# Optimization experiments

Hardware: AMD Instinct MI355X
Metric: run time of the kernel (lower is better)

Reference implementation:

```python
import jax, jax.numpy as jnp
import numpy as np

N, E = 50000, 800000        # nodes, edges
L, MUL, S = 2, 32, 5        # layers, irrep multiplicity, num_species
NB, H = 8, 64               # num_bessel, radial MLP hidden
R_MAX = 5.0
AVG_NEIGH = 16.0
NW = 4 * MUL                # radial-MLP output size: 4 uvu TP paths x mul


def _envelope(x, p=6):
    # polynomial cutoff envelope u(x), smoothly -> 0 at x=1
    u = (1.0
         - (p + 1.0) * (p + 2.0) / 2.0 * x ** p
         + p * (p + 2.0) * x ** (p + 1)
         - p * (p + 1.0) / 2.0 * x ** (p + 2))
    return u * (x < 1.0)


def _forward(edge_vectors, node_species, senders, receivers, embed_w,
             w_res_s, w_res_v, w_lin1_s, w_lin1_v, mlp_w0, mlp_w1, mlp_w2,
             w_lin2_s, w_lin2_v, w_out1, w_out2):
    r = jnp.sqrt(jnp.sum(edge_vectors ** 2, -1) + 1e-12)            # [E] safe_norm
    unit = edge_vectors / r[:, None]
    sh1 = jnp.sqrt(3.0) * unit                                      # l=1 SH, component norm [E,3]
    # Bessel radial basis * polynomial envelope -> edge embedding [E,NB]
    n = jnp.arange(1, NB + 1, dtype=jnp.float32)
    bessel = jnp.sqrt(2.0 / R_MAX) * jnp.sin(n[None, :] * jnp.pi * r[:, None] / R_MAX) / r[:, None]
    edge_embedded = bessel * _envelope(r / R_MAX)[:, None]

    onehot = jax.nn.one_hot(node_species, S, dtype=jnp.float32)     # [N,S] node attrs (Sx0e)
    h_s = (onehot @ embed_w) / jnp.sqrt(S)                          # [N,MUL] 0e features
    h_v = jnp.zeros((N, MUL, 3), jnp.float32)                       # [N,MUL,3] 1o features (no path from 0e attrs)

    for l in range(L):
        # residual: FullyConnectedTensorProduct(node_feats, node_attrs) into h_out irreps
        res_s = jnp.einsum('nu,ns,usk->nk', h_s, onehot, w_res_s[l]) / jnp.sqrt(MUL * S)   # [N,2*MUL] (feat+gate scalars)
        res_v = jnp.einsum('nui,ns,usv->nvi', h_v, onehot, w_res_v[l]) / jnp.sqrt(MUL * S) # [N,MUL,3]
        # self-interaction Linear (per-irrep channel mixing)
        hs = (h_s @ w_lin1_s[l]) / jnp.sqrt(MUL)
        hv = jnp.einsum('nui,uv->nvi', h_v, w_lin1_v[l]) / jnp.sqrt(MUL)
        # gather sender node features onto edges
        es, ev = hs[senders], hv[senders]                           # [E,MUL], [E,MUL,3]
        # radial MLP (swish, no bias) -> per-edge uvu TP path weights [E, 4*MUL]
        a = jax.nn.silu(edge_embedded @ (mlp_w0[l] / jnp.sqrt(NB)))
        a = jax.nn.silu(a @ (mlp_w1[l] / jnp.sqrt(H)))
        w = a @ mlp_w2[l]
        w1, w2, w3, w4 = jnp.split(w, 4, axis=-1)
        # per-edge Clebsch-Gordan tensor product, uvu mode, radial weights
        o0a = w1 * es                                               # 0e x 0e -> 0e
        o0b = w2 * jnp.einsum('eui,ei->eu', ev, sh1) / jnp.sqrt(3.0)  # 1o x 1o -> 0e
        o1a = (w3 * es)[:, :, None] * sh1[:, None, :]               # 0e x 1o -> 1o
        o1b = w4[:, :, None] * ev                                   # 1o x 0e -> 1o
        # scatter-sum to receiver nodes + neighbor normalization
        seg = lambda x: jax.ops.segment_sum(x, receivers, num_segments=N) / AVG_NEIGH
        n0 = jnp.concatenate([seg(o0a), seg(o0b)], axis=-1)         # [N,2*MUL]
        n1 = jnp.concatenate([seg(o1a), seg(o1b)], axis=1)          # [N,2*MUL,3]
        # Linear to h_out irreps, add residual
        s_out = n0 @ w_lin2_s[l] / jnp.sqrt(2 * MUL) + res_s        # [N,2*MUL]
        v_out = jnp.einsum('nui,uv->nvi', n1, w_lin2_v[l]) / jnp.sqrt(2 * MUL) + res_v
        # gated nonlinearity: swish on even scalars, swish-activated gates scale vectors
        h_s = jax.nn.silu(s_out[:, :MUL])
        h_v = v_out * jax.nn.silu(s_out[:, MUL:])[:, :, None]
    # scalar readout: MUL -> MUL//2 -> 1 per node
    z = (h_s @ w_out1) / jnp.sqrt(MUL)
    e_node = (z @ w_out2) / jnp.sqrt(MUL // 2)
    return jnp.ravel(e_node)                                        # [N]


def setup_inputs():
    key = jax.random.key(0)
    ks = jax.random.split(key, 16)
    return {
        "edge_vectors": jax.random.normal(ks[0], (E, 3), jnp.float32) * 2.0,
        "node_species": jax.random.randint(ks[1], (N,), 0, S),
        "senders": jax.random.randint(ks[2], (E,), 0, N),
        "receivers": jax.random.randint(ks[3], (E,), 0, N),
        "embed_w": jax.random.normal(ks[4], (S, MUL), jnp.float32),
        "w_res_s": jax.random.normal(ks[5], (L, MUL, S, 2 * MUL), jnp.float32),
        "w_res_v": jax.random.normal(ks[6], (L, MUL, S, MUL), jnp.float32),
        "w_lin1_s": jax.random.normal(ks[7], (L, MUL, MUL), jnp.float32),
        "w_lin1_v": jax.random.normal(ks[8], (L, MUL, MUL), jnp.float32),
        "mlp_w0": jax.random.normal(ks[9], (L, NB, H), jnp.float32) * 4.0,
        "mlp_w1": jax.random.normal(ks[10], (L, H, H), jnp.float32) * 4.0,
        "mlp_w2": jax.random.normal(ks[11], (L, H, NW), jnp.float32) * 4.0 / np.sqrt(H),
        "w_lin2_s": jax.random.normal(ks[12], (L, 2 * MUL, 2 * MUL), jnp.float32),
        "w_lin2_v": jax.random.normal(ks[13], (L, 2 * MUL, MUL), jnp.float32),
        "w_out1": jax.random.normal(ks[14], (MUL, MUL // 2), jnp.float32),
        "w_out2": jax.random.normal(ks[15], (MUL // 2, 1), jnp.float32),
    }


def reference(edge_vectors, node_species, senders, receivers, embed_w,
              w_res_s, w_res_v, w_lin1_s, w_lin1_v, mlp_w0, mlp_w1, mlp_w2,
              w_lin2_s, w_lin2_v, w_out1, w_out2):
    return _forward(edge_vectors, node_species, senders, receivers, embed_w,
                    w_res_s, w_res_v, w_lin1_s, w_lin1_v, mlp_w0, mlp_w1, mlp_w2,
                    w_lin2_s, w_lin2_v, w_out1, w_out2)
```

## Files before the change

kernel.cpp:

```cpp
#include <hip/hip_runtime.h>
#include <math.h>

#define NN 50000
#define EE 800000
#define TB 4096

typedef float f32x2 __attribute__((ext_vector_type(2)));
typedef float f32x4  __attribute__((ext_vector_type(4)));

__device__ __forceinline__ float silu_f(float x) {
    return x / (1.f + __expf(-x));
}

__global__ __launch_bounds__(256) void k_table(
        const float* __restrict__ mlp_w0, const float* __restrict__ mlp_w1,
        const float* __restrict__ mlp_w2,
        float* __restrict__ tab0, float* __restrict__ tab1) {
    __shared__ float stage[4][128];
    int wv = threadIdx.x >> 6, lane = threadIdx.x & 63;
    int wid = blockIdx.x * 4 + wv;
    if (wid > 2 * TB + 1) wid = 2 * TB + 1;
    int l = wid / (TB + 1);
    int bin = wid - l * (TB + 1);
    float* st = stage[wv];

    float r = 5.f * (float)bin / (float)TB;
    if (r < 1e-6f) r = 1e-6f;
    float ir = 1.f / r;
    float xx = r * 0.2f;
    float env = 0.f;
    if (xx < 1.f) {
        float x2 = xx * xx, x3 = x2 * xx, x6 = x3 * x3, x7 = x6 * xx, x8 = x7 * xx;
        env = 1.f - 28.f * x6 + 48.f * x7 - 21.f * x8;
    }
    float coef = 0.6324555320336759f * env * ir;
    const float w5 = 0.6283185307179586f;

    float p = 0.f;
#pragma unroll
    for (int k = 0; k < 8; ++k)
        p += coef * __sinf(w5 * (float)(k + 1) * r) * mlp_w0[l * 512 + k * 64 + lane];
    float a1 = silu_f(p * 0.35355339059327373f);
    st[lane] = a1;
    __syncthreads();
    float q = 0.f;
    for (int j = 0; j < 64; ++j) q += st[j] * mlp_w1[l * 4096 + j * 64 + lane];
    float a2 = silu_f(q * 0.125f);
    __syncthreads();
    st[lane] = a2;
    __syncthreads();
    float wlo = 0.f, whi = 0.f;
    for (int h = 0; h < 64; ++h) {
        float a = st[h];
        wlo += a * mlp_w2[l * 8192 + h * 128 + lane];
        whi += a * mlp_w2[l * 8192 + h * 128 + 64 + lane];
    }
    __syncthreads();
    st[lane] = wlo;
    st[64 + lane] = whi;
    __syncthreads();
    if (lane < 16) {
        f32x4 o;
        if (l == 0) {
            o[0] = st[lane]; o[1] = st[64 + lane];
            o[2] = st[16 + lane]; o[3] = st[80 + lane];
            ((f32x4*)tab0)[bin * 16 + lane] = o;
        } else {
            o[0] = st[lane]; o[1] = st[32 + lane];
            o[2] = st[16 + lane]; o[3] = st[48 + lane];
            ((f32x4*)tab1)[bin * 16 + lane] = o;
        }
    }
}

__global__ void k_fs(const float* __restrict__ embed_w, const float* __restrict__ w_lin1_s,
                     float* __restrict__ fs) {
    int t = threadIdx.x;
    if (t >= 160) return;
    int sp = t >> 5, v = t & 31;
    float acc = 0.f;
#pragma unroll
    for (int u = 0; u < 32; ++u) acc += embed_w[sp * 32 + u] * w_lin1_s[u * 32 + v];
    fs[t] = acc * 0.4472135954999579f * 0.17677669529663687f;
}

__global__ void k_hist(const int* __restrict__ recv, int* __restrict__ deg) {
    int e = blockIdx.x * 256 + threadIdx.x;
    if (e < EE) atomicAdd(&deg[recv[e]], 1);
}

__global__ void k_scan(const int* __restrict__ deg, int* __restrict__ row_start,
                       int* __restrict__ cursor) {
    __shared__ int part[256];
    int t = threadIdx.x;
    int lo = t * 196, hi = lo + 196 > NN ? NN : lo + 196;
    int s = 0;
    for (int i = lo; i < hi; ++i) s += deg[i];
    part[t] = s;
    __syncthreads();
    for (int d = 1; d < 256; d <<= 1) {
        int add = (t >= d) ? part[t - d] : 0;
        __syncthreads();
        part[t] += add;
        __syncthreads();
    }
    int run = part[t] - s;
    for (int i = lo; i < hi; ++i) {
        row_start[i] = run;
        cursor[i] = run;
        run += deg[i];
    }
    if (t == 255) row_start[NN] = run;
}

__global__ void k_fill(const int* __restrict__ recv, const int* __restrict__ senders,
                       const int* __restrict__ species, const float* __restrict__ evec,
                       int* __restrict__ cursor,
                       int* __restrict__ csr_send, int* __restrict__ csr_recv,
                       float* __restrict__ ev3) {
    int e = blockIdx.x * 256 + threadIdx.x;
    if (e >= EE) return;
    int rv = recv[e];
    int p = atomicAdd(&cursor[rv], 1);
    int snd = senders[e];
    csr_send[p] = snd | (species[snd] << 24);
    csr_recv[p] = rv;
    ev3[p * 3 + 0] = evec[e * 3 + 0];
    ev3[p * 3 + 1] = evec[e * 3 + 1];
    ev3[p * 3 + 2] = evec[e * 3 + 2];
}

#define WROWS 20
#define WSTRIDE 260
template<int L>
__global__ __launch_bounds__(256) void k_mega(
    const int* __restrict__ csr_send, const int* __restrict__ csr_recv,
    const float* __restrict__ ev3, const int* __restrict__ row_start,
    const float* __restrict__ fs, const float* __restrict__ feat,
    const float* __restrict__ tab,
    float* __restrict__ n0, float* __restrict__ n1) {
    __shared__ f32x4 accw4[WROWS * WSTRIDE / 4];
    __shared__ f32x4 lds_esh[256];
    __shared__ float lds_x[256];
    __shared__ int lds_wd[256];
    __shared__ int sh_base, sh_last;
    float* accw = (float*)accw4;

    int tid = threadIdx.x;
    int p0 = blockIdx.x * 256;
    int lane = tid & 63;
    int wv = tid >> 6;
    int c0 = lane & 15;
    int rg = lane >> 4;

    for (int i = tid; i < WROWS * WSTRIDE / 4; i += 256) accw4[i] = (f32x4)0.f;

    int sndp = csr_send[p0 + tid];
    int rv = csr_recv[p0 + tid];
    if (tid == 0)   sh_base = rv;
    if (tid == 255) sh_last = rv;
    {
        float x = ev3[(p0 + tid) * 3 + 0], y = ev3[(p0 + tid) * 3 + 1], z = ev3[(p0 + tid) * 3 + 2];
        float r = sqrtf(x * x + y * y + z * z + 1e-12f);
        float ir = 1.f / r;
        const float s3 = 1.7320508075688772f;
        f32x4 esh;
        esh[0] = s3 * x * ir;
        esh[1] = s3 * y * ir;
        esh[2] = s3 * z * ir;
        esh[3] = __int_as_float(sndp);
        lds_esh[tid] = esh;
        float xb = r * ((float)TB / 5.f);
        if (xb > (float)TB) xb = (float)TB;
        lds_x[tid] = xb;
    }
    __syncthreads();
    int node_base = sh_base;
    lds_wd[tid] = rv - node_base;

    const f32x4* tabv = (const f32x4*)tab;
    const f32x4* feat4 = (const f32x4*)feat;
    const float rs3 = 0.5773502691896258f;

    for (int t = 0; t < 4; ++t) {
        int tOff = wv * 64 + t * 16;

        f32x4 eshv[4], dv[4];
        int wr[4];
        float es0[4], es1[4];
#pragma unroll
        for (int j = 0; j < 4; ++j) {
            int idx = tOff + rg * 4 + j;
            eshv[j] = lds_esh[idx];
            wr[j] = lds_wd[idx];
            float xb = lds_x[idx];
            int bin = (int)xb;
            if (bin >= TB) bin = TB - 1;
            float fr = xb - (float)bin;
            f32x4 lo = tabv[bin * 16 + c0];
            f32x4 hi = tabv[bin * 16 + 16 + c0];
            dv[j] = lo + fr * (hi - lo);
            if (L == 0) {
                int sp = ((unsigned)__float_as_int(eshv[j][3])) >> 24;
                es0[j] = fs[sp * 32 + c0];
                es1[j] = fs[sp * 32 + 16 + c0];
            }
        }

#pragma unroll
        for (int b = 0; b < 2; ++b) {
            int u = b * 16 + c0;
            float s0 = 0.f, s1 = 0.f, s2 = 0.f, s3v = 0.f;
            int curw = wr[0];
            auto emit = [&](int wrow) {
                if (L == 0) {
                    if (wrow < WROWS) {
                        float* arow = accw + wrow * WSTRIDE;
                        atomicAdd(arow + u, s0);
                        atomicAdd(arow + 64 + u, s1);
                        atomicAdd(arow + 128 + u, s2);
                        atomicAdd(arow + 192 + u, s3v);
                    } else {
                        int rvn = node_base + wrow;
                        atomicAdd(n0 + (size_t)rvn * 64 + u, s0);
                        atomicAdd(n1 + (size_t)rvn * 192 + u, s1);
                        atomicAdd(n1 + (size_t)rvn * 192 + 64 + u, s2);
                        atomicAdd(n1 + (size_t)rvn * 192 + 128 + u, s3v);
                    }
                } else {
                    if (wrow < WROWS) {
                        float* arow = accw + wrow * WSTRIDE;
                        atomicAdd(arow + u, s0);
                        atomicAdd(arow + 32 + u, s1);
                    } else {
                        int rvn = node_base + wrow;
                        atomicAdd(n0 + (size_t)rvn * 64 + u, s0);
                        atomicAdd(n0 + (size_t)rvn * 64 + 32 + u, s1);
                    }
                }
            };
#pragma unroll
            for (int j = 0; j < 4; ++j) {
                int wrow = wr[j];
                if (j > 0 && wrow != curw) {
                    emit(curw);
                    s0 = s1 = s2 = s3v = 0.f;
                    curw = wrow;
                }
                f32x4 esh = eshv[j];
                float dA = dv[j][2 * b];
                float dB = dv[j][2 * b + 1];
                if (L == 0) {
                    float es = b ? es1[j] : es0[j];
                    float t3 = dB * es;
                    s0  += dA * es;
                    s1  += t3 * esh[0];
                    s2  += t3 * esh[1];
                    s3v += t3 * esh[2];
                } else {
                    int s = __float_as_int(esh[3]) & 0xFFFFFF;
                    f32x4 f4 = feat4[(size_t)s * 32 + u];
                    float dot = f4[1] * esh[0] + f4[2] * esh[1] + f4[3] * esh[2];
                    s0 += dA * f4[0];
                    s1 += dB * dot * rs3;
                }
            }
            int alive = 1;
            {
                int pw = __shfl_xor(curw, 16);
                float t0 = __shfl_xor(s0, 16), t1 = __shfl_xor(s1, 16);
                float t2 = __shfl_xor(s2, 16), t3m = __shfl_xor(s3v, 16);
                if (pw == curw) {
                    s0 += t0; s1 += t1;
                    if (L == 0) { s2 += t2; s3v += t3m; }
                    if (lane & 16) alive = 0;
                }
            }
            {
                int pw = __shfl_xor(curw, 32);
                int pal = __shfl_xor(alive, 32);
                float t0 = __shfl_xor(s0, 32), t1 = __shfl_xor(s1, 32);
                float t2 = __shfl_xor(s2, 32), t3m = __shfl_xor(s3v, 32);
                if (alive && pal && pw == curw) {
                    s0 += t0; s1 += t1;
                    if (L == 0) { s2 += t2; s3v += t3m; }
                    if (lane & 32) alive = 0;
                }
            }
            if (alive) emit(curw);
        }
    }
    __syncthreads();

    int span = sh_last - node_base;
    if (span > WROWS - 1) span = WROWS - 1;
    for (int wl = 0; wl <= span; ++wl) {
        int n = node_base + wl;
        float v = accw[wl * WSTRIDE + tid];
        bool interior = (row_start[n] >= p0) && (row_start[n + 1] <= p0 + 256);
        if (L == 1) {
            if (tid < 64) {
                float* dest = n0 + (size_t)n * 64 + tid;
                if (interior) *dest = v;
                else if (v != 0.f) atomicAdd(dest, v);
            }
        } else {
            float* dest = (tid < 64) ? (n0 + (size_t)n * 64 + tid) : (n1 + (size_t)n * 192 + (tid - 64));
            if (interior) *dest = v;
            else if (v != 0.f) atomicAdd(dest, v);
        }
    }
}

__global__ __launch_bounds__(256) void k_upd0_prep(
        const int* __restrict__ species,
        const float* __restrict__ n0, const float* __restrict__ n1,
        const float* __restrict__ w_lin2_s, const float* __restrict__ w_lin2_v,
        const float* __restrict__ w_res_s, const float* __restrict__ embed_w,
        const float* __restrict__ w_lin1_s, const float* __restrict__ w_lin1_v,
        float* __restrict__ h_s, float* __restrict__ feat) {
    __shared__ float stage[4][128];
    int lane = threadIdx.x & 63;
    int wv = threadIdx.x >> 6;
    int n = blockIdx.x * 4 + wv;
    n = __builtin_amdgcn_readfirstlane(n);
    int sp = __builtin_amdgcn_readfirstlane(species[n]);
    const float sc_l2 = 1.f / 128.f;
    const float rr = 0.07905694150420949f * 0.4472135954999579f;

    const float* n0r = n0 + (size_t)n * 64;
    float sk = 0.f;
#pragma unroll 8
    for (int j = 0; j < 64; ++j)
        sk += n0r[j] * w_lin2_s[j * 64 + lane];
    sk *= sc_l2;
#pragma unroll 8
    for (int u = 0; u < 32; ++u)
        sk += (embed_w[sp * 32 + u] * rr) * w_res_s[(u * 5 + sp) * 64 + lane];
    float act = silu_f(sk);
    float gmine = __shfl(act, 32 + (lane & 31));

    const float* n1r = n1 + (size_t)n * 192;
    int i0 = lane >> 5, v = lane & 31;
    float acc0 = 0.f, acc2 = 0.f;
#pragma unroll 8
    for (int u = 0; u < 32; ++u) {
        float wlv = w_lin2_v[u * 32 + v];
        acc0 += n1r[i0 * 64 + u] * wlv;
        acc2 += n1r[128 + u] * wlv;
    }
    float* st = stage[wv];
    st[32 + i0 * 32 + v] = acc0 * sc_l2 * gmine;
    if (lane < 32) {
        st[v] = act;
        st[96 + v] = acc2 * sc_l2 * gmine;
        h_s[(size_t)n * 32 + v] = act;
    }
    __syncthreads();

    const float rs32 = 0.17677669529663687f;
    float accA = 0.f, accB = 0.f;
#pragma unroll 8
    for (int u = 0; u < 32; ++u) {
        float wsv = w_lin1_s[u * 32 + v];
        float wvv = w_lin1_v[u * 32 + v];
        float xs = st[u];
        float xx = st[32 + u];
        float xy = st[64 + u];
        float xz = st[96 + u];
        float inA = i0 ? xy : xs;
        float wA  = i0 ? wvv : wsv;
        float inB = i0 ? xz : xx;
        accA += inA * wA;
        accB += inB * wvv;
    }
    f32x2 o;
    o[0] = accA * rs32;
    o[1] = accB * rs32;
    *(f32x2*)(feat + (size_t)n * 128 + v * 4 + i0 * 2) = o;
}

__global__ __launch_bounds__(256) void k_node_update_last(
        const int* __restrict__ species,
        const float* __restrict__ n0,
        const float* __restrict__ w_lin2_s, const float* __restrict__ w_res_s,
        const float* __restrict__ h_s,
        const float* __restrict__ w_out1, const float* __restrict__ w_out2,
        float* __restrict__ out) {
    int lane = threadIdx.x & 63;
    int n = blockIdx.x * 4 + (threadIdx.x >> 6);
    n = __builtin_amdgcn_readfirstlane(n);
    if (n >= NN) return;
    if (lane >= 32) return;
    int sp = __builtin_amdgcn_readfirstlane(species[n]);
    const float sc_l2 = 1.f / 128.f;
    const float rs160 = 0.07905694150420949f;

    const float* n0r = n0 + (size_t)n * 64;
    float sk = 0.f;
#pragma unroll 8
    for (int j = 0; j < 64; ++j)
        sk += n0r[j] * w_lin2_s[j * 64 + lane];
    sk *= sc_l2;
    const float* hsr = h_s + (size_t)n * 32;
#pragma unroll 8
    for (int u = 0; u < 32; ++u)
        sk += (hsr[u] * rs160) * w_res_s[(u * 5 + sp) * 64 + lane];
    float act = silu_f(sk);

    float wc = 0.f;
#pragma unroll
    for (int j = 0; j < 16; ++j)
        wc += w_out1[lane * 16 + j] * w_out2[j];
    float e = act * wc;
    e += __shfl_xor(e, 1);
    e += __shfl_xor(e, 2);
    e += __shfl_xor(e, 4);
    e += __shfl_xor(e, 8);
    e += __shfl_xor(e, 16);
    if (lane == 0)
        out[n] = e * 0.17677669529663687f * 0.25f;
}

extern "C" void kernel_launch(void* const* d_in, const int* in_sizes, int n_in,
                              void* d_out, int out_size, void* d_ws, size_t ws_size,
                              hipStream_t stream) {
    const float* evec     = (const float*)d_in[0];
    const int*   species  = (const int*)d_in[1];
    const int*   senders  = (const int*)d_in[2];
    const int*   receivers= (const int*)d_in[3];
    const float* embed_w  = (const float*)d_in[4];
    const float* w_res_s  = (const float*)d_in[5];
    const float* w_res_v  = (const float*)d_in[6];
    const float* w_lin1_s = (const float*)d_in[7];
    const float* w_lin1_v = (const float*)d_in[8];
    const float* mlp_w0   = (const float*)d_in[9];
    const float* mlp_w1   = (const float*)d_in[10];
    const float* mlp_w2   = (const float*)d_in[11];
    const float* w_lin2_s = (const float*)d_in[12];
    const float* w_lin2_v = (const float*)d_in[13];
    const float* w_out1   = (const float*)d_in[14];
    const float* w_out2   = (const float*)d_in[15];
    (void)w_res_v;

    float* ws = (float*)d_ws;
    size_t off = 0;
    auto alloc = [&](size_t n) { float* p = ws + off; off += (n + 3) & ~(size_t)3; return p; };

    float* h_s  = alloc(NN * 32);
    float* feat = alloc((size_t)NN * 128);
    float* n0b  = alloc(NN * 64);
    float* n1b  = alloc(NN * 192);
    float* tab0 = alloc((size_t)(TB + 1) * 64);
    float* tab1 = alloc((size_t)(TB + 1) * 64);
    float* fs   = alloc(160);
    int*   deg       = (int*)alloc(NN);
    int*   row_start = (int*)alloc(NN + 1);
    int*   cursor    = (int*)alloc(NN);
    int*   csr_send  = (int*)alloc(EE);
    int*   csr_recv  = (int*)alloc(EE);
    float* ev3       = alloc((size_t)EE * 3);

    k_table<<<(2 * (TB + 1) + 3) / 4, 256, 0, stream>>>(mlp_w0, mlp_w1, mlp_w2, tab0, tab1);
    k_fs<<<1, 256, 0, stream>>>(embed_w, w_lin1_s, fs);

    hipMemsetAsync(deg, 0, NN * 4, stream);
    k_hist<<<(EE + 255) / 256, 256, 0, stream>>>(receivers, deg);
    k_scan<<<1, 256, 0, stream>>>(deg, row_start, cursor);
    k_fill<<<(EE + 255) / 256, 256, 0, stream>>>(receivers, senders, species, evec,
                                                 cursor, csr_send, csr_recv, ev3);

    hipMemsetAsync(n0b, 0, (size_t)NN * 256 * 4, stream);
    k_mega<0><<<EE / 256, 256, 0, stream>>>(
        csr_send, csr_recv, ev3, row_start, fs, feat, tab0, n0b, n1b);
    k_upd0_prep<<<12500, 256, 0, stream>>>(
        species, n0b, n1b, w_lin2_s, w_lin2_v, w_res_s, embed_w,
        w_lin1_s + 1024, w_lin1_v + 1024, h_s, feat);

    hipMemsetAsync(n0b, 0, (size_t)NN * 64 * 4, stream);
    k_mega<1><<<EE / 256, 256, 0, stream>>>(
        csr_send, csr_recv, ev3, row_start, fs, feat, tab1, n0b, n1b);
    k_node_update_last<<<12500, 256, 0, stream>>>(
        species, n0b, w_lin2_s + 4096, w_res_s + 10240, h_s,
        w_out1, w_out2, (float*)d_out);
}
```

Measured before the change: 569.9 us.

## Fuse small setup kernels, precompute edge geometry in fill, trim mega reductions

Folds the species-feature kernel into the table kernel and merges the degree memset into the n0/n1 memset, cutting launch count. k_fill now computes the unit vectors and the table coordinate and stores them as one aligned float4 per edge, so both mega kernels load precomputed geometry instead of recomputing it. k_scan reads degrees with int4 loads. The mega kernel drops the xor-32 cross-half reduction stage, skips the extra shuffles when L=1, and shrinks the LDS accumulator. The risk is correctness: the dropped reduction stage and smaller WROWS must still cover each block's receiver span, and the removed bounds check in the last kernel is only safe because NN is a multiple of 4.

New measurement: 559.0 us. Within noise of the previous version (-1.9%).

```diff
diff --git a/kernel.cpp b/kernel.cpp
--- a/kernel.cpp
+++ b/kernel.cpp
@@ -15,13 +15,14 @@
 __global__ __launch_bounds__(256) void k_table(
         const float* __restrict__ mlp_w0, const float* __restrict__ mlp_w1,
         const float* __restrict__ mlp_w2,
-        float* __restrict__ tab0, float* __restrict__ tab1) {
+        const float* __restrict__ embed_w, const float* __restrict__ w_lin1_s,
+        float* __restrict__ tab0, float* __restrict__ tab1, float* __restrict__ fs) {
     __shared__ float stage[4][128];
     int wv = threadIdx.x >> 6, lane = threadIdx.x & 63;
     int wid = blockIdx.x * 4 + wv;
-    if (wid > 2 * TB + 1) wid = 2 * TB + 1;
-    int l = wid / (TB + 1);
-    int bin = wid - l * (TB + 1);
+    int widc = wid > 2 * TB + 1 ? 2 * TB + 1 : wid;
+    int l = widc / (TB + 1);
+    int bin = widc - l * (TB + 1);
     float* st = stage[wv];
 
     float r = 5.f * (float)bin / (float)TB;
@@ -59,7 +60,7 @@
     st[lane] = wlo;
     st[64 + lane] = whi;
     __syncthreads();
-    if (lane < 16) {
+    if (wid <= 2 * TB + 1 && lane < 16) {
         f32x4 o;
         if (l == 0) {
             o[0] = st[lane]; o[1] = st[64 + lane];
@@ -71,17 +72,14 @@
             ((f32x4*)tab1)[bin * 16 + lane] = o;
         }
     }
-}
-
-__global__ void k_fs(const float* __restrict__ embed_w, const float* __restrict__ w_lin1_s,
-                     float* __restrict__ fs) {
-    int t = threadIdx.x;
-    if (t >= 160) return;
-    int sp = t >> 5, v = t & 31;
-    float acc = 0.f;
-#pragma unroll
-    for (int u = 0; u < 32; ++u) acc += embed_w[sp * 32 + u] * w_lin1_s[u * 32 + v];
-    fs[t] = acc * 0.4472135954999579f * 0.17677669529663687f;
+    int ft = (wid - (2 * TB + 2)) * 64 + lane;
+    if (wid >= 2 * TB + 2 && ft < 160) {
+        int sp = ft >> 5, v = ft & 31;
+        float acc = 0.f;
+#pragma unroll
+        for (int u = 0; u < 32; ++u) acc += embed_w[sp * 32 + u] * w_lin1_s[u * 32 + v];
+        fs[ft] = acc * 0.4472135954999579f * 0.17677669529663687f;
+    }
 }
 
 __global__ void k_hist(const int* __restrict__ recv, int* __restrict__ deg) {
@@ -95,7 +93,13 @@
     int t = threadIdx.x;
     int lo = t * 196, hi = lo + 196 > NN ? NN : lo + 196;
     int s = 0;
-    for (int i = lo; i < hi; ++i) s += deg[i];
+    if (t < 255) {
+        const int4* d4 = (const int4*)(deg + lo);
+#pragma unroll 7
+        for (int i = 0; i < 49; ++i) { int4 v = d4[i]; s += v.x + v.y + v.z + v.w; }
+    } else {
+        for (int i = lo; i < hi; ++i) s += deg[i];
+    }
     part[t] = s;
     __syncthreads();
     for (int d = 1; d < 256; d <<= 1) {
@@ -117,7 +121,7 @@
                        const int* __restrict__ species, const float* __restrict__ evec,
                        int* __restrict__ cursor,
                        int* __restrict__ csr_send, int* __restrict__ csr_recv,
-                       float* __restrict__ ev3) {
+                       float* __restrict__ ev4) {
     int e = blockIdx.x * 256 + threadIdx.x;
     if (e >= EE) return;
     int rv = recv[e];
@@ -125,17 +129,26 @@
     int snd = senders[e];
     csr_send[p] = snd | (species[snd] << 24);
     csr_recv[p] = rv;
-    ev3[p * 3 + 0] = evec[e * 3 + 0];
-    ev3[p * 3 + 1] = evec[e * 3 + 1];
-    ev3[p * 3 + 2] = evec[e * 3 + 2];
-}
-
-#define WROWS 20
-#define WSTRIDE 260
+    float x = evec[e * 3 + 0], y = evec[e * 3 + 1], z = evec[e * 3 + 2];
+    float r = sqrtf(x * x + y * y + z * z + 1e-12f);
+    float ir = 1.f / r;
+    const float s3 = 1.7320508075688772f;
+    float xb = r * ((float)TB / 5.f);
+    if (xb > (float)TB) xb = (float)TB;
+    f32x4 o;
+    o[0] = s3 * x * ir;
+    o[1] = s3 * y * ir;
+    o[2] = s3 * z * ir;
+    o[3] = xb;
+    *(f32x4*)(ev4 + (size_t)p * 4) = o;
+}
+
+#define WROWS 18
+#define WSTRIDE 256
 template<int L>
 __global__ __launch_bounds__(256) void k_mega(
     const int* __restrict__ csr_send, const int* __restrict__ csr_recv,
-    const float* __restrict__ ev3, const int* __restrict__ row_start,
+    const float* __restrict__ ev4, const int* __restrict__ row_start,
     const float* __restrict__ fs, const float* __restrict__ feat,
     const float* __restrict__ tab,
     float* __restrict__ n0, float* __restrict__ n1) {
@@ -160,19 +173,12 @@
     if (tid == 0)   sh_base = rv;
     if (tid == 255) sh_last = rv;
     {
-        float x = ev3[(p0 + tid) * 3 + 0], y = ev3[(p0 + tid) * 3 + 1], z = ev3[(p0 + tid) * 3 + 2];
-        float r = sqrtf(x * x + y * y + z * z + 1e-12f);
-        float ir = 1.f / r;
-        const float s3 = 1.7320508075688772f;
+        f32x4 g = *(const f32x4*)(ev4 + (size_t)(p0 + tid) * 4);
         f32x4 esh;
-        esh[0] = s3 * x * ir;
-        esh[1] = s3 * y * ir;
-        esh[2] = s3 * z * ir;
+        esh[0] = g[0]; esh[1] = g[1]; esh[2] = g[2];
         esh[3] = __int_as_float(sndp);
         lds_esh[tid] = esh;
-        float xb = r * ((float)TB / 5.f);
-        if (xb > (float)TB) xb = (float)TB;
-        lds_x[tid] = xb;
+        lds_x[tid] = g[3];
     }
     __syncthreads();
     int node_base = sh_base;
@@ -265,29 +271,19 @@
                     s1 += dB * dot * rs3;
                 }
             }
-            int alive = 1;
             {
                 int pw = __shfl_xor(curw, 16);
                 float t0 = __shfl_xor(s0, 16), t1 = __shfl_xor(s1, 16);
-                float t2 = __shfl_xor(s2, 16), t3m = __shfl_xor(s3v, 16);
+                float t2 = 0.f, t3m = 0.f;
+                if (L == 0) { t2 = __shfl_xor(s2, 16); t3m = __shfl_xor(s3v, 16); }
+                bool alive = true;
                 if (pw == curw) {
                     s0 += t0; s1 += t1;
                     if (L == 0) { s2 += t2; s3v += t3m; }
-                    if (lane & 16) alive = 0;
+                    if (lane & 16) alive = false;
                 }
+                if (alive) emit(curw);
             }
-            {
-                int pw = __shfl_xor(curw, 32);
-                int pal = __shfl_xor(alive, 32);
-                float t0 = __shfl_xor(s0, 32), t1 = __shfl_xor(s1, 32);
-                float t2 = __shfl_xor(s2, 32), t3m = __shfl_xor(s3v, 32);
-                if (alive && pal && pw == curw) {
-                    s0 += t0; s1 += t1;
-                    if (L == 0) { s2 += t2; s3v += t3m; }
-                    if (lane & 32) alive = 0;
-                }
-            }
-            if (alive) emit(curw);
         }
     }
     __syncthreads();
@@ -390,7 +386,6 @@
     int lane = threadIdx.x & 63;
     int n = blockIdx.x * 4 + (threadIdx.x >> 6);
     n = __builtin_amdgcn_readfirstlane(n);
-    if (n >= NN) return;
     if (lane >= 32) return;
     int sp = __builtin_amdgcn_readfirstlane(species[n]);
     const float sc_l2 = 1.f / 128.f;
@@ -451,35 +446,33 @@
     float* feat = alloc((size_t)NN * 128);
     float* n0b  = alloc(NN * 64);
     float* n1b  = alloc(NN * 192);
+    int*   deg  = (int*)alloc(NN);
     float* tab0 = alloc((size_t)(TB + 1) * 64);
     float* tab1 = alloc((size_t)(TB + 1) * 64);
     float* fs   = alloc(160);
-    int*   deg       = (int*)alloc(NN);
     int*   row_start = (int*)alloc(NN + 1);
     int*   cursor    = (int*)alloc(NN);
     int*   csr_send  = (int*)alloc(EE);
     int*   csr_recv  = (int*)alloc(EE);
-    float* ev3       = alloc((size_t)EE * 3);
-
-    k_table<<<(2 * (TB + 1) + 3) / 4, 256, 0, stream>>>(mlp_w0, mlp_w1, mlp_w2, tab0, tab1);
-    k_fs<<<1, 256, 0, stream>>>(embed_w, w_lin1_s, fs);
-
-    hipMemsetAsync(deg, 0, NN * 4, stream);
+    float* ev4       = alloc((size_t)EE * 4);
+
+    hipMemsetAsync(n0b, 0, (size_t)NN * 257 * 4, stream);
+    k_table<<<(2 * (TB + 1) + 3 + 3) / 4, 256, 0, stream>>>(
+        mlp_w0, mlp_w1, mlp_w2, embed_w, w_lin1_s, tab0, tab1, fs);
     k_hist<<<(EE + 255) / 256, 256, 0, stream>>>(receivers, deg);
     k_scan<<<1, 256, 0, stream>>>(deg, row_start, cursor);
     k_fill<<<(EE + 255) / 256, 256, 0, stream>>>(receivers, senders, species, evec,
-                                                 cursor, csr_send, csr_recv, ev3);
-
-    hipMemsetAsync(n0b, 0, (size_t)NN * 256 * 4, stream);
+                                                 cursor, csr_send, csr_recv, ev4);
+
     k_mega<0><<<EE / 256, 256, 0, stream>>>(
-        csr_send, csr_recv, ev3, row_start, fs, feat, tab0, n0b, n1b);
+        csr_send, csr_recv, ev4, row_start, fs, feat, tab0, n0b, n1b);
     k_upd0_prep<<<12500, 256, 0, stream>>>(
         species, n0b, n1b, w_lin2_s, w_lin2_v, w_res_s, embed_w,
         w_lin1_s + 1024, w_lin1_v + 1024, h_s, feat);
 
     hipMemsetAsync(n0b, 0, (size_t)NN * 64 * 4, stream);
     k_mega<1><<<EE / 256, 256, 0, stream>>>(
-        csr_send, csr_recv, ev3, row_start, fs, feat, tab1, n0b, n1b);
+        csr_send, csr_recv, ev4, row_start, fs, feat, tab1, n0b, n1b);
     k_node_update_last<<<12500, 256, 0, stream>>>(
         species, n0b, w_lin2_s + 4096, w_res_s + 10240, h_s,
         w_out1, w_out2, (float*)d_out);
```
